# Optimization experiments

Hardware: AMD Instinct MI355X
Metric: run time of the kernel (lower is better)

## Reference

```python
import jax, jax.numpy as jnp
import numpy as np

D = 1024      # embed_dim
H = 16        # num_heads
HD = D // H   # head_dim


def setup_inputs() -> dict:
    key = jax.random.key(0)
    ks = jax.random.split(key, 9)
    s = 0.02
    x = jax.random.normal(ks[0], (8, 1024, D), dtype=jnp.float32)
    # Per-head Q/K/V linears, torch Linear layout [out, in] -> stacked [H, HD, D]
    Wq = jax.random.normal(ks[1], (H, HD, D), dtype=jnp.float32) * s
    Wk = jax.random.normal(ks[2], (H, HD, D), dtype=jnp.float32) * s
    Wv = jax.random.normal(ks[3], (H, HD, D), dtype=jnp.float32) * s
    bq = jax.random.normal(ks[4], (H, HD), dtype=jnp.float32) * s
    bk = jax.random.normal(ks[5], (H, HD), dtype=jnp.float32) * s
    bv = jax.random.normal(ks[6], (H, HD), dtype=jnp.float32) * s
    Wo = jax.random.normal(ks[7], (D, D), dtype=jnp.float32) * s
    bo = jax.random.normal(ks[8], (D,), dtype=jnp.float32) * s
    return {"x": x, "Wq": Wq, "Wk": Wk, "Wv": Wv,
            "bq": bq, "bk": bk, "bv": bv, "Wo": Wo, "bo": bo}


def reference(x, Wq, Wk, Wv, bq, bk, bv, Wo, bo):
    # Batched per-head projections: [B,S,D] x [H,HD,D] -> [B,H,S,HD]
    q = jnp.einsum('bsd,hkd->bhsk', x, Wq) + bq[None, :, None, :]
    k = jnp.einsum('bsd,hkd->bhsk', x, Wk) + bk[None, :, None, :]
    v = jnp.einsum('bsd,hkd->bhsk', x, Wv) + bv[None, :, None, :]
    scores = jnp.einsum('bhqk,bhsk->bhqs', q, k) / jnp.sqrt(jnp.float32(HD))
    probs = jax.nn.softmax(scores, axis=-1)          # [B,H,S,S]
    attn = jnp.einsum('bhqs,bhsk->bhqk', probs, v)   # [B,H,S,HD]
    # Concat heads along feature dim -> [B,S,D]
    B, _, S, _ = attn.shape
    concat = jnp.transpose(attn, (0, 2, 1, 3)).reshape(B, S, D)
    out = jnp.einsum('bsd,ed->bse', concat, Wo) + bo  # output projection
    return out
```

## Files before the change

### kernel.cpp

```cpp
#include <hip/hip_runtime.h>
#include <stdint.h>
#include <stddef.h>


typedef short bf16x8 __attribute__((ext_vector_type(8)));
typedef float f32x4  __attribute__((ext_vector_type(4)));
typedef unsigned short u16x8 __attribute__((ext_vector_type(8)));
typedef unsigned short u16x4 __attribute__((ext_vector_type(4)));

#define MFMA16 __builtin_amdgcn_mfma_f32_16x16x32_bf16

typedef const void __attribute__((address_space(1)))* gas1_t;
typedef void __attribute__((address_space(3)))* las3_t;

static __device__ __forceinline__ void gload16(const void* g, void* l) {
  __builtin_amdgcn_global_load_lds((gas1_t)g, (las3_t)l, 16, 0, 0);
}

static __device__ __forceinline__ unsigned short f2bf(float f) {
  union { float f; unsigned int u; } v; v.f = f;
  unsigned int r = v.u + 0x7fffu + ((v.u >> 16) & 1u);
  return (unsigned short)(r >> 16);
}

__global__ __launch_bounds__(256) void cast_all(
    const float* __restrict__ x, const float* __restrict__ Wq,
    const float* __restrict__ Wk, const float* __restrict__ Wv,
    const float* __restrict__ Wo,
    unsigned short* __restrict__ xb, unsigned short* __restrict__ wqkv,
    unsigned short* __restrict__ wob) {
  int base = (blockIdx.x * 256 + threadIdx.x) * 4;
  const float* s; unsigned short* d;
  if (base < 8388608) { s = x + base; d = xb + base; }
  else if (base < 11534336) {
    int o = base - 8388608; int wi = o >> 20;
    const float* w = (wi == 0) ? Wq : (wi == 1) ? Wk : Wv;
    s = w + (o & 1048575); d = wqkv + o;
  } else {
    int o = base - 11534336; s = Wo + o; d = wob + o;
  }
  float4 f = *(const float4*)s;
  u16x4 r; r[0] = f2bf(f.x); r[1] = f2bf(f.y); r[2] = f2bf(f.z); r[3] = f2bf(f.w);
  *(u16x4*)d = r;
}

template <int EPI>
__global__ __launch_bounds__(256) void gemm128(
    const unsigned short* __restrict__ A, const unsigned short* __restrict__ Bm,
    float* __restrict__ Cf, const float* __restrict__ bO,
    unsigned short* __restrict__ Qo, unsigned short* __restrict__ Ko,
    unsigned short* __restrict__ Vo,
    const float* __restrict__ bq, const float* __restrict__ bk,
    const float* __restrict__ bv) {
  __shared__ __align__(16) char sm[32768];
  char* As = sm; char* Bs = sm + 16384;
  const int tid = threadIdx.x, lane = tid & 63, w = tid >> 6;
  const int wr = w >> 1, wc = w & 1;
  const int brow = blockIdx.y * 128, bcol = blockIdx.x * 128;
  const int l15 = lane & 15, g = lane >> 4;
  f32x4 acc[4][4] = {};
  for (int ks = 0; ks < 16; ++ks) {
    __syncthreads();
#pragma unroll
    for (int j = 0; j < 4; ++j) {
      int p = (w * 4 + j) * 1024 + lane * 16;
      int row = p >> 7;
      int cl = (lane & 7) ^ (row & 7);
      gload16(A + (size_t)(brow + row) * 1024 + ks * 64 + cl * 8,
              As + (w * 4 + j) * 1024);
      gload16(Bm + (size_t)(bcol + row) * 1024 + ks * 64 + cl * 8,
              Bs + (w * 4 + j) * 1024);
    }
    asm volatile("s_waitcnt vmcnt(0)" ::: "memory");
    __syncthreads();
#pragma unroll
    for (int kk = 0; kk < 2; ++kk) {
      bf16x8 af[4], bfr[4];
#pragma unroll
      for (int mi = 0; mi < 4; ++mi) {
        int row = wr * 64 + mi * 16 + l15;
        int off = (row * 128 + kk * 64 + g * 16) ^ ((row & 7) << 4);
        af[mi] = *(const bf16x8*)(As + off);
      }
#pragma unroll
      for (int ni = 0; ni < 4; ++ni) {
        int row = wc * 64 + ni * 16 + l15;
        int off = (row * 128 + kk * 64 + g * 16) ^ ((row & 7) << 4);
        bfr[ni] = *(const bf16x8*)(Bs + off);
      }
#pragma unroll
      for (int mi = 0; mi < 4; ++mi)
#pragma unroll
        for (int ni = 0; ni < 4; ++ni)
          acc[mi][ni] = MFMA16(af[mi], bfr[ni], acc[mi][ni], 0, 0, 0);
    }
  }
  if constexpr (EPI == 0) {
    const int b = brow >> 10;
#pragma unroll
    for (int ni = 0; ni < 4; ++ni) {
      int n = bcol + wc * 64 + ni * 16 + l15;
      int t = n >> 10, nh = n & 1023;
      int h = nh >> 6, hd = nh & 63;
      const float* bias = (t == 0) ? bq : (t == 1) ? bk : bv;
      float bb = bias[nh];
      if (t == 2) {
        size_t vtb = ((size_t)(b * 16 + h) * 64 + hd) * 1024;
#pragma unroll
        for (int mi = 0; mi < 4; ++mi) {
          int m0 = brow + wr * 64 + mi * 16 + g * 4;
          int srow0 = m0 & 1023;
          u16x4 vv;
#pragma unroll
          for (int r = 0; r < 4; ++r) vv[r] = f2bf(acc[mi][ni][r] + bb);
          *(u16x4*)(Vo + vtb + srow0) = vv;
        }
      } else {
        float scale = (t == 0) ? 0.125f : 1.0f;
        unsigned short* dst = (t == 0) ? Qo : Ko;
        size_t basei = ((size_t)(b * 16 + h) * 1024) * 64 + hd;
#pragma unroll
        for (int mi = 0; mi < 4; ++mi)
#pragma unroll
          for (int r = 0; r < 4; ++r) {
            int m = brow + wr * 64 + mi * 16 + g * 4 + r;
            int srow = m & 1023;
            dst[basei + (size_t)srow * 64] = f2bf((acc[mi][ni][r] + bb) * scale);
          }
      }
    }
  } else {
#pragma unroll
    for (int ni = 0; ni < 4; ++ni) {
      int n = bcol + wc * 64 + ni * 16 + l15;
      float bb = bO[n];
#pragma unroll
      for (int mi = 0; mi < 4; ++mi)
#pragma unroll
        for (int r = 0; r < 4; ++r) {
          int m = brow + wr * 64 + mi * 16 + g * 4 + r;
          Cf[(size_t)m * 1024 + n] = acc[mi][ni][r] + bb;
        }
    }
  }
}

__global__ __launch_bounds__(256, 3) void attn_fused(
    const unsigned short* __restrict__ Qb, const unsigned short* __restrict__ Kb,
    const unsigned short* __restrict__ VtG, unsigned short* __restrict__ Cc) {
  __shared__ __align__(16) char sm[49152];
  char* Ks = sm;
  char* Vt = sm + 16384;
  const int tid = threadIdx.x, lane = tid & 63, w = tid >> 6;
  char* Ps = sm + 32768 + w * 4096;
  const int l15 = lane & 15, g = lane >> 4;
  const int id = blockIdx.x;
  const int qt = id >> 7, bh = id & 127;
  const size_t hb = (size_t)bh * (1024 * 64);

  bf16x8 qreg[2][2];
#pragma unroll
  for (int kk = 0; kk < 2; ++kk)
#pragma unroll
    for (int ni = 0; ni < 2; ++ni) {
      int q = qt * 128 + w * 32 + ni * 16 + l15;
      qreg[kk][ni] = *(const bf16x8*)(Qb + hb + (size_t)q * 64 + kk * 32 + g * 8);
    }

  auto stage = [&](int c, int buf) {
#pragma unroll
    for (int j = 0; j < 2; ++j) {
      int p = (w * 2 + j) * 1024 + lane * 16;
      int row = p >> 7;
      int cl = (lane & 7) ^ (row & 7);
      gload16(Kb + hb + (size_t)(c * 64 + row) * 64 + cl * 8,
              Ks + buf * 8192 + (w * 2 + j) * 1024);
      gload16(VtG + hb + (size_t)row * 1024 + c * 64 + cl * 8,
              Vt + buf * 8192 + (w * 2 + j) * 1024);
    }
  };

  stage(0, 0);
  asm volatile("s_waitcnt vmcnt(0)" ::: "memory");
  __syncthreads();

  f32x4 acc[4][2] = {};
  float m_run[2] = {-1e30f, -1e30f};
  float l_run[2] = {0.f, 0.f};

  for (int c = 0; c < 16; ++c) {
    const int cur = c & 1;
    if (c < 15) stage(c + 1, cur ^ 1);
    const char* Kc = Ks + cur * 8192;
    const char* Vc = Vt + cur * 8192;

    f32x4 st[4][2] = {};
#pragma unroll
    for (int kk = 0; kk < 2; ++kk) {
      bf16x8 ka[4];
#pragma unroll
      for (int mi = 0; mi < 4; ++mi) {
        int row = mi * 16 + l15;
        int off = (row * 128 + kk * 64 + g * 16) ^ ((row & 7) << 4);
        ka[mi] = *(const bf16x8*)(Kc + off);
      }
#pragma unroll
      for (int mi = 0; mi < 4; ++mi)
#pragma unroll
        for (int ni = 0; ni < 2; ++ni)
          st[mi][ni] = MFMA16(ka[mi], qreg[kk][ni], st[mi][ni], 0, 0, 0);
    }

    float corr_s[2];
#pragma unroll
    for (int ni = 0; ni < 2; ++ni) {
      float mx = -1e30f;
#pragma unroll
      for (int mi = 0; mi < 4; ++mi)
#pragma unroll
        for (int r = 0; r < 4; ++r) mx = fmaxf(mx, st[mi][ni][r]);
      mx = fmaxf(mx, __shfl_xor(mx, 16));
      mx = fmaxf(mx, __shfl_xor(mx, 32));
      float mn = fmaxf(m_run[ni], mx);
      float corr = __expf(m_run[ni] - mn);
      float sum = 0.f;
      const int q = ni * 16 + l15;
      const int rbase = q * 128, sw = (q & 7) << 4;
#pragma unroll
      for (int mi = 0; mi < 4; ++mi) {
        u16x4 pk;
#pragma unroll
        for (int r = 0; r < 4; ++r) {
          float e = __expf(st[mi][ni][r] - mn);
          sum += e;
          pk[r] = f2bf(e);
        }
        *(u16x4*)(Ps + ((rbase + (mi * 16 + g * 4) * 2) ^ sw)) = pk;
      }
      sum += __shfl_xor(sum, 16);
      sum += __shfl_xor(sum, 32);
      l_run[ni] = l_run[ni] * corr + sum;
      m_run[ni] = mn;
      corr_s[ni] = corr;
    }

#pragma unroll
    for (int nd = 0; nd < 4; ++nd)
#pragma unroll
      for (int ni = 0; ni < 2; ++ni)
#pragma unroll
        for (int r = 0; r < 4; ++r)
          acc[nd][ni][r] *= corr_s[ni];

#pragma unroll
    for (int kk = 0; kk < 2; ++kk) {
      bf16x8 vf[4], pa[2];
#pragma unroll
      for (int nd = 0; nd < 4; ++nd) {
        int row = nd * 16 + l15;
        int off = (row * 128 + kk * 64 + g * 16) ^ ((row & 7) << 4);
        vf[nd] = *(const bf16x8*)(Vc + off);
      }
#pragma unroll
      for (int ni = 0; ni < 2; ++ni) {
        int q = ni * 16 + l15;
        int off = (q * 128 + kk * 64 + g * 16) ^ ((q & 7) << 4);
        pa[ni] = *(const bf16x8*)(Ps + off);
      }
#pragma unroll
      for (int nd = 0; nd < 4; ++nd)
#pragma unroll
        for (int ni = 0; ni < 2; ++ni)
          acc[nd][ni] = MFMA16(vf[nd], pa[ni], acc[nd][ni], 0, 0, 0);
    }

    asm volatile("s_waitcnt vmcnt(0)" ::: "memory");
    __syncthreads();
  }

  const int b = bh >> 4, h = bh & 15;
  float invl[2] = {1.f / l_run[0], 1.f / l_run[1]};
#pragma unroll
  for (int ni = 0; ni < 2; ++ni) {
    int q = qt * 128 + w * 32 + ni * 16 + l15;
    size_t rowb = (size_t)(b * 1024 + q) * 1024 + h * 64;
#pragma unroll
    for (int nd = 0; nd < 4; ++nd) {
      u16x4 o;
#pragma unroll
      for (int r = 0; r < 4; ++r) o[r] = f2bf(acc[nd][ni][r] * invl[ni]);
      *(u16x4*)(Cc + rowb + nd * 16 + g * 4) = o;
    }
  }
}

extern "C" void kernel_launch(void* const* d_in, const int* in_sizes, int n_in,
                              void* d_out, int out_size, void* d_ws, size_t ws_size,
                              hipStream_t stream) {
  const float* x  = (const float*)d_in[0];
  const float* Wq = (const float*)d_in[1];
  const float* Wk = (const float*)d_in[2];
  const float* Wv = (const float*)d_in[3];
  const float* bq = (const float*)d_in[4];
  const float* bk = (const float*)d_in[5];
  const float* bv = (const float*)d_in[6];
  const float* Wo = (const float*)d_in[7];
  const float* bo = (const float*)d_in[8];

  char* ws = (char*)d_ws;
  unsigned short* xb   = (unsigned short*)(ws);
  unsigned short* wqkv = (unsigned short*)(ws + 16777216);
  unsigned short* wob  = (unsigned short*)(ws + 23068672);
  unsigned short* Qb   = (unsigned short*)(ws + 25165824);
  unsigned short* Kb   = (unsigned short*)(ws + 41943040);
  unsigned short* VtG  = (unsigned short*)(ws + 58720256);
  unsigned short* Cc   = xb;

  cast_all<<<dim3(12288), dim3(256), 0, stream>>>(x, Wq, Wk, Wv, Wo, xb, wqkv, wob);
  gemm128<0><<<dim3(24, 64), dim3(256), 0, stream>>>(
      xb, wqkv, nullptr, nullptr, Qb, Kb, VtG, bq, bk, bv);
  attn_fused<<<dim3(1024), dim3(256), 0, stream>>>(Qb, Kb, VtG, Cc);
  gemm128<1><<<dim3(8, 64), dim3(256), 0, stream>>>(
      Cc, wob, (float*)d_out, bo, nullptr, nullptr, nullptr, nullptr, nullptr, nullptr);
}
```

Measured before the change: 255.7 us.

## Double-buffer GEMM LDS tiles and swizzle block order for QKV projection

```diff
diff --git a/kernel.cpp b/kernel.cpp
--- a/kernel.cpp
+++ b/kernel.cpp
@@ -44,7 +44,7 @@
   *(u16x4*)d = r;
 }
 
-template <int EPI>
+template <int EPI, int NBX, bool SWZ>
 __global__ __launch_bounds__(256) void gemm128(
     const unsigned short* __restrict__ A, const unsigned short* __restrict__ Bm,
     float* __restrict__ Cf, const float* __restrict__ bO,
@@ -52,27 +52,40 @@
     unsigned short* __restrict__ Vo,
     const float* __restrict__ bq, const float* __restrict__ bk,
     const float* __restrict__ bv) {
-  __shared__ __align__(16) char sm[32768];
-  char* As = sm; char* Bs = sm + 16384;
+  __shared__ __align__(16) char sm[65536];
   const int tid = threadIdx.x, lane = tid & 63, w = tid >> 6;
   const int wr = w >> 1, wc = w & 1;
-  const int brow = blockIdx.y * 128, bcol = blockIdx.x * 128;
+  int i = blockIdx.x, j;
+  if constexpr (SWZ) j = (i & 7) * (NBX * 64 / 8) + (i >> 3);
+  else j = i;
+  const int bcol = (j % NBX) * 128, brow = (j / NBX) * 128;
   const int l15 = lane & 15, g = lane >> 4;
-  f32x4 acc[4][4] = {};
-  for (int ks = 0; ks < 16; ++ks) {
-    __syncthreads();
-#pragma unroll
-    for (int j = 0; j < 4; ++j) {
-      int p = (w * 4 + j) * 1024 + lane * 16;
+
+  auto stage = [&](int ks, int buf) {
+    char* Ad = sm + buf * 32768;
+    char* Bd = Ad + 16384;
+#pragma unroll
+    for (int jj = 0; jj < 4; ++jj) {
+      int p = (w * 4 + jj) * 1024 + lane * 16;
       int row = p >> 7;
       int cl = (lane & 7) ^ (row & 7);
       gload16(A + (size_t)(brow + row) * 1024 + ks * 64 + cl * 8,
-              As + (w * 4 + j) * 1024);
+              Ad + (w * 4 + jj) * 1024);
       gload16(Bm + (size_t)(bcol + row) * 1024 + ks * 64 + cl * 8,
-              Bs + (w * 4 + j) * 1024);
-    }
-    asm volatile("s_waitcnt vmcnt(0)" ::: "memory");
-    __syncthreads();
+              Bd + (w * 4 + jj) * 1024);
+    }
+  };
+
+  stage(0, 0);
+  asm volatile("s_waitcnt vmcnt(0)" ::: "memory");
+  __syncthreads();
+
+  f32x4 acc[4][4] = {};
+  for (int ks = 0; ks < 16; ++ks) {
+    const int cur = ks & 1;
+    if (ks < 15) stage(ks + 1, cur ^ 1);
+    const char* As = sm + cur * 32768;
+    const char* Bs = As + 16384;
 #pragma unroll
     for (int kk = 0; kk < 2; ++kk) {
       bf16x8 af[4], bfr[4];
@@ -94,6 +107,8 @@
         for (int ni = 0; ni < 4; ++ni)
           acc[mi][ni] = MFMA16(af[mi], bfr[ni], acc[mi][ni], 0, 0, 0);
     }
+    asm volatile("s_waitcnt vmcnt(0)" ::: "memory");
+    __syncthreads();
   }
   if constexpr (EPI == 0) {
     const int b = brow >> 10;
@@ -317,9 +332,9 @@
   unsigned short* Cc   = xb;
 
   cast_all<<<dim3(12288), dim3(256), 0, stream>>>(x, Wq, Wk, Wv, Wo, xb, wqkv, wob);
-  gemm128<0><<<dim3(24, 64), dim3(256), 0, stream>>>(
+  gemm128<0, 24, true><<<dim3(1536), dim3(256), 0, stream>>>(
       xb, wqkv, nullptr, nullptr, Qb, Kb, VtG, bq, bk, bv);
   attn_fused<<<dim3(1024), dim3(256), 0, stream>>>(Qb, Kb, VtG, Cc);
-  gemm128<1><<<dim3(8, 64), dim3(256), 0, stream>>>(
+  gemm128<1, 8, false><<<dim3(512), dim3(256), 0, stream>>>(
       Cc, wob, (float*)d_out, bo, nullptr, nullptr, nullptr, nullptr, nullptr, nullptr);
 }
```

Result: no change. 252.6 us (-1.2%).
